# Optimization experiments

Measured on AMD Instinct MI355X. Metric: run time of the kernel, lower is better.

The kernel has to match this reference:

```python
import jax, jax.numpy as jnp
import numpy as np

B, S, D, H = 2, 2048, 1024, 16
DH = D // H          # 64, even -> RoPE valid
ROPE_BASE = 10000.0
LN_EPS = 1e-5


def _rope_cache(seq_len, head_dim, dtype):
    half = head_dim // 2
    inv_freq = 1.0 / (ROPE_BASE ** (jnp.arange(half, dtype=jnp.float32) / half))
    t = jnp.arange(seq_len, dtype=jnp.float32)
    freqs = t[:, None] * inv_freq[None, :]            # [S, half]
    emb = jnp.concatenate([freqs, freqs], axis=-1)    # [S, DH]
    return jnp.cos(emb).astype(dtype)[None, None], jnp.sin(emb).astype(dtype)[None, None]


def _rotate_every_two(x):
    x_even = x[..., ::2]
    x_odd = x[..., 1::2]
    return jnp.stack([-x_odd, x_even], axis=-1).reshape(x.shape)


def setup_inputs() -> dict:
    key = jax.random.key(0)
    ks = jax.random.split(key, 4)
    w = lambda k, shape: (jax.random.normal(k, shape, jnp.float32) * 0.02)
    return {
        "x_qk": jax.random.normal(ks[0], (B, S, D), jnp.float32),
        "x_v": jax.random.normal(ks[1], (B, S, D), jnp.float32),
        "W_qk": w(ks[2], (D, 2 * D)),
        "b_qk": jnp.zeros((2 * D,), jnp.float32),
        "W_v": w(ks[3], (D, D)),
        "b_v": jnp.zeros((D,), jnp.float32),
        "ln_gamma": jnp.ones((D,), jnp.float32),
        "ln_beta": jnp.zeros((D,), jnp.float32),
    }


def reference(x_qk, x_v, W_qk, b_qk, W_v, b_v, ln_gamma, ln_beta):
    b, s, d = x_qk.shape
    # fused QK projection -> [B,S,2,H,DH]
    qk = (x_qk @ W_qk + b_qk).reshape(b, s, 2, H, DH)
    q = jnp.transpose(qk[:, :, 0], (0, 2, 1, 3))  # [B,H,S,DH]
    k = jnp.transpose(qk[:, :, 1], (0, 2, 1, 3))
    v = jnp.transpose((x_v @ W_v + b_v).reshape(b, s, H, DH), (0, 2, 1, 3))

    cos, sin = _rope_cache(s, DH, q.dtype)
    q = q * cos + _rotate_every_two(q) * sin
    k = k * cos + _rotate_every_two(k) * sin

    scale = 1.0 / jnp.sqrt(jnp.asarray(DH, q.dtype))
    scores = jnp.einsum("bhqd,bhkd->bhqk", q, k) * scale
    probs = jax.nn.softmax(scores, axis=-1)
    attn = jnp.einsum("bhqk,bhkd->bhqd", probs, v)      # [B,H,S,DH]
    attn = jnp.transpose(attn, (0, 2, 1, 3)).reshape(b, s, d)

    mu = jnp.mean(attn, axis=-1, keepdims=True)
    var = jnp.var(attn, axis=-1, keepdims=True)
    out = (attn - mu) * jax.lax.rsqrt(var + LN_EPS) * ln_gamma + ln_beta
    return out
```

## Files before the change

kernel.cpp:

```cpp
#include <hip/hip_runtime.h>
#include <hip/hip_bf16.h>

#define Bn 2
#define Sn 2048
#define Dn 1024
#define Hn 16
#define DHn 64
#define Kd 1024
#define Mn (Bn * Sn)
#define LN10K 9.210340371976184f

typedef __attribute__((ext_vector_type(8))) short bf16x8;
typedef __attribute__((ext_vector_type(4))) float f32x4;
typedef __attribute__((ext_vector_type(16))) float f32x16;

static __device__ __forceinline__ ushort f2bf(float f) {
    uint u = __float_as_uint(f);
    u += 0x7fff + ((u >> 16) & 1);
    return (ushort)(u >> 16);
}
static __device__ __forceinline__ uint cvtpk(float a, float b) {
    uint r;
    asm("v_cvt_pk_bf16_f32 %0, %1, %2" : "=v"(r) : "v"(a), "v"(b));
    return r;
}
static __device__ __forceinline__ void plswap(uint& a, uint& b) {
    asm volatile("v_permlane32_swap_b32 %0, %1" : "+v"(a), "+v"(b));
}

#define MFMA16(a, b, c) __builtin_amdgcn_mfma_f32_16x16x32_bf16((a), (b), (c), 0, 0, 0)
#define MFMA32(a, b, c) __builtin_amdgcn_mfma_f32_32x32x16_bf16((a), (b), (c), 0, 0, 0)

static __device__ __forceinline__ void gload16(const ushort* g, ushort* l) {
    __builtin_amdgcn_global_load_lds(
        (const __attribute__((address_space(1))) void*)g,
        (__attribute__((address_space(3))) void*)l, 16, 0, 0);
}

static __device__ __forceinline__ int swz(int row, int col16) {
    return row * 128 + (((col16) * 16) ^ ((row & 7) << 4));
}

__global__ __launch_bounds__(256) void prep(
    const float* __restrict__ x_qk, const float* __restrict__ x_v,
    const float* __restrict__ W_qk, const float* __restrict__ W_v,
    ushort* __restrict__ xqkB, ushort* __restrict__ xvB,
    ushort* __restrict__ WqkT, ushort* __restrict__ WvT,
    float* __restrict__ ct, float* __restrict__ st)
{
    __shared__ ushort tle[32][33];
    const int blk = blockIdx.x;
    const int tid = threadIdx.x;

    if (blk < 4096) {
        const float* in = (blk < 2048) ? x_qk : x_v;
        ushort* out = (blk < 2048) ? xqkB : xvB;
        const int lb = (blk < 2048) ? blk : blk - 2048;
        const size_t i = ((size_t)lb * 256 + tid) * 8;
        const float4 a = *(const float4*)(in + i);
        const float4 b = *(const float4*)(in + i + 4);
        *(ushort4*)(out + i) =
            make_ushort4(f2bf(a.x), f2bf(a.y), f2bf(a.z), f2bf(a.w));
        *(ushort4*)(out + i + 4) =
            make_ushort4(f2bf(b.x), f2bf(b.y), f2bf(b.z), f2bf(b.w));
    } else if (blk < 7168) {
        const bool isQK = blk < 6144;
        const int t = isQK ? blk - 4096 : blk - 6144;
        const int C = isQK ? 2048 : 1024;
        const float* in = isQK ? W_qk : W_v;
        ushort* out = isQK ? WqkT : WvT;
        const int n0 = (isQK ? (t & 63) : (t & 31)) * 32;
        const int k0 = (isQK ? (t >> 6) : (t >> 5)) * 32;
        const int x = tid & 31, y = tid >> 5;
#pragma unroll
        for (int i = 0; i < 4; ++i)
            tle[y + 8 * i][x] = f2bf(in[(size_t)(k0 + y + 8 * i) * C + n0 + x]);
        __syncthreads();
#pragma unroll
        for (int i = 0; i < 4; ++i)
            out[(size_t)(n0 + y + 8 * i) * Kd + k0 + x] = tle[x][y + 8 * i];
    } else {
        const int idx = (blk - 7168) * 256 + tid;
        const int s = idx >> 5, fe = idx & 31;
        const float f = expf(-LN10K * (float)fe / 32.0f);
        const float a = (float)s * f;
        ct[idx] = cosf(a);
        st[idx] = sinf(a);
    }
}

__global__ __launch_bounds__(256) void gemm_fused_all(
    const ushort* __restrict__ xqkB, const ushort* __restrict__ xvB,
    const ushort* __restrict__ WqkT, const ushort* __restrict__ WvT,
    const float* __restrict__ b_qk, const float* __restrict__ b_v,
    const float* __restrict__ ctab, const float* __restrict__ stab,
    ushort* __restrict__ Qw, ushort* __restrict__ Kw, ushort* __restrict__ Vtw)
{
    __shared__ ushort Asm[128 * 64];
    __shared__ ushort Bsm[128 * 64];

    const bool isQK = blockIdx.x < 16;
    const ushort* A  = isQK ? xqkB : xvB;
    const ushort* Bt = isQK ? WqkT : WvT;
    const float* bias = isQK ? b_qk : b_v;
    const int nbase = (isQK ? blockIdx.x : blockIdx.x - 16) * 128;
    const int mbase = blockIdx.y * 128;

    const int tid = threadIdx.x;
    const int lane = tid & 63, w = tid >> 6;
    const int g = lane >> 4, c = lane & 15;
    const int wm = (w >> 1) * 64, wn = (w & 1) * 64;

    f32x4 acc[4][4];
#pragma unroll
    for (int mf = 0; mf < 4; ++mf)
#pragma unroll
        for (int nf = 0; nf < 4; ++nf)
            acc[mf][nf] = (f32x4){0.f, 0.f, 0.f, 0.f};

    const int sbase = w * 64 + lane;

    for (int k0 = 0; k0 < Kd; k0 += 64) {
#pragma unroll
        for (int j = 0; j < 4; ++j) {
            const int i = j * 256 + sbase;
            const int row = i >> 3, c16 = i & 7;
            const int kc = (c16 ^ (row & 7)) * 8;
            gload16(A + (size_t)(mbase + row) * Kd + k0 + kc,
                    &Asm[(size_t)(j * 256 + w * 64) * 8]);
            gload16(Bt + (size_t)(nbase + row) * Kd + k0 + kc,
                    &Bsm[(size_t)(j * 256 + w * 64) * 8]);
        }
        __syncthreads();

#pragma unroll
        for (int ks = 0; ks < 2; ++ks) {
            bf16x8 af[4], bfr[4];
#pragma unroll
            for (int mf = 0; mf < 4; ++mf) {
                const int row = wm + mf * 16 + c;
                af[mf] = *(const bf16x8*)((const char*)Asm + swz(row, ks * 4 + g));
            }
#pragma unroll
            for (int nf = 0; nf < 4; ++nf) {
                const int row = wn + nf * 16 + c;
                bfr[nf] = *(const bf16x8*)((const char*)Bsm + swz(row, ks * 4 + g));
            }
#pragma unroll
            for (int mf = 0; mf < 4; ++mf)
#pragma unroll
                for (int nf = 0; nf < 4; ++nf)
                    acc[mf][nf] = MFMA16(af[mf], bfr[nf], acc[mf][nf]);
        }
        __syncthreads();
    }

#pragma unroll
    for (int nf = 0; nf < 4; ++nf) {
        const int col = nbase + wn + nf * 16 + c;
        const float bs = bias[col];
        if (isQK) {
            const int dh = col & 63, h = (col >> 6) & 15, isK = col >> 10;
            ushort* dst = isK ? Kw : Qw;
            const float sc = isK ? 1.0f : 0.18033688011112042f;
            const float* cr = ctab + (dh & 31);
            const float* sr = stab + (dh & 31);
#pragma unroll
            for (int mf = 0; mf < 4; ++mf) {
#pragma unroll
                for (int r = 0; r < 4; ++r) {
                    const int row = mbase + wm + mf * 16 + g * 4 + r;
                    const int s = row & 2047, b = row >> 11;
                    const float v = acc[mf][nf][r] + bs;
                    const float p = __shfl_xor(v, 1);
                    const float cs = cr[s * 32], sn = sr[s * 32];
                    const float ov = (c & 1) ? v * cs + p * sn
                                             : v * cs - p * sn;
                    dst[(((size_t)(b * Hn + h)) * Sn + s) * DHn + dh] =
                        f2bf(ov * sc);
                }
            }
        } else {
            const int h = col >> 6, dh = col & 63;
#pragma unroll
            for (int mf = 0; mf < 4; ++mf) {
#pragma unroll
                for (int r = 0; r < 4; ++r) {
                    const int row = mbase + wm + mf * 16 + g * 4 + r;
                    const int s = row & 2047, b = row >> 11;
                    const float v = acc[mf][nf][r] + bs;
                    Vtw[(((size_t)(b * Hn + h)) * DHn + dh) * Sn + s] = f2bf(v);
                }
            }
        }
    }
}

__global__ __launch_bounds__(256) void attn_mfma(
    const ushort* __restrict__ Qg, const ushort* __restrict__ Kg,
    const ushort* __restrict__ Vtg, float* __restrict__ Aw)
{
    __shared__ char Kt[3][8192];
    __shared__ char Vt[3][8192];

    const int tid = threadIdx.x;
    const int lane = tid & 63, w = tid >> 6;
    const int r31 = lane & 31, hi = lane >> 5;
    const int bh = blockIdx.y;
    const int b = bh >> 4, h = bh & 15;
    const int q0 = blockIdx.x * 128 + w * 32;

    const ushort* qp = Qg + ((size_t)bh * Sn + q0 + r31) * DHn + hi * 8;
    bf16x8 qf[4];
#pragma unroll
    for (int kt = 0; kt < 4; ++kt)
        qf[kt] = *(const bf16x8*)(qp + kt * 16);

    const ushort* Kb = Kg + (size_t)bh * Sn * DHn;
    const ushort* Vb = Vtg + (size_t)bh * DHn * Sn;

    auto stage = [&](int buf, int kb) {
#pragma unroll
        for (int j = 0; j < 2; ++j) {
            const int i = j * 256 + w * 64 + lane;
            const int row = i >> 3, c16 = i & 7;
            const int kc = (c16 ^ (row & 7)) * 8;
            gload16(Kb + (size_t)(kb + row) * DHn + kc,
                    (ushort*)&Kt[buf][(j * 256 + w * 64) * 16]);
            gload16(Vb + (size_t)row * Sn + kb + kc,
                    (ushort*)&Vt[buf][(j * 256 + w * 64) * 16]);
        }
    };

    stage(0, 0);
    stage(1, 64);

    f32x16 acc0, acc1;
#pragma unroll
    for (int i = 0; i < 16; ++i) { acc0[i] = 0.f; acc1[i] = 0.f; }
    float m = -1e30f, lp = 0.f;

    const int NT = Sn / 64;
    for (int t = 0; t < NT; ++t) {
        const int cur = t % 3;

        if (t < NT - 1) {
            asm volatile("s_waitcnt vmcnt(4)" ::: "memory");
        } else {
            asm volatile("s_waitcnt vmcnt(0)" ::: "memory");
        }
        __builtin_amdgcn_sched_barrier(0);
        __builtin_amdgcn_s_barrier();
        __builtin_amdgcn_sched_barrier(0);

        f32x16 C0, C1;
#pragma unroll
        for (int i = 0; i < 16; ++i) { C0[i] = 0.f; C1[i] = 0.f; }
        __builtin_amdgcn_s_setprio(1);
#pragma unroll
        for (int kt = 0; kt < 4; ++kt) {
            const bf16x8 ka = *(const bf16x8*)&Kt[cur][swz(r31, kt * 2 + hi)];
            C0 = MFMA32(ka, qf[kt], C0);
        }
#pragma unroll
        for (int kt = 0; kt < 4; ++kt) {
            const bf16x8 ka = *(const bf16x8*)&Kt[cur][swz(32 + r31, kt * 2 + hi)];
            C1 = MFMA32(ka, qf[kt], C1);
        }
        __builtin_amdgcn_s_setprio(0);

        float mx[8];
#pragma unroll
        for (int i = 0; i < 8; ++i)
            mx[i] = fmaxf(fmaxf(C0[i], C0[i + 8]), fmaxf(C1[i], C1[i + 8]));
        mx[0] = fmaxf(mx[0], mx[4]); mx[1] = fmaxf(mx[1], mx[5]);
        mx[2] = fmaxf(mx[2], mx[6]); mx[3] = fmaxf(mx[3], mx[7]);
        float pmax = fmaxf(fmaxf(mx[0], mx[1]), fmaxf(mx[2], mx[3]));
        pmax = fmaxf(pmax, __shfl_xor(pmax, 32));

        if (__any(pmax > m + 11.5f)) {
            const float mn = fmaxf(m, pmax);
            const float a = exp2f(m - mn);
            m = mn;
            lp *= a;
#pragma unroll
            for (int reg = 0; reg < 16; ++reg) {
                const int qr = (reg & 3) + 8 * (reg >> 2) + 4 * hi;
                const float ar = __shfl(a, qr);
                acc0[reg] *= ar;
                acc1[reg] *= ar;
            }
        }

        bf16x8 paf[4];
#pragma unroll
        for (int tile = 0; tile < 2; ++tile) {
            const f32x16& C = tile ? C1 : C0;
            float e[16];
#pragma unroll
            for (int i = 0; i < 16; ++i) e[i] = exp2f(C[i] - m);
            float s = 0.f;
#pragma unroll
            for (int i = 0; i < 16; ++i) s += e[i];
            lp += s;
            uint p01 = cvtpk(e[0], e[1]),  p23 = cvtpk(e[2], e[3]);
            uint p45 = cvtpk(e[4], e[5]),  p67 = cvtpk(e[6], e[7]);
            uint p89 = cvtpk(e[8], e[9]),  pab = cvtpk(e[10], e[11]);
            uint pcd = cvtpk(e[12], e[13]), pef = cvtpk(e[14], e[15]);
            plswap(p01, p45); plswap(p23, p67);
            plswap(p89, pcd); plswap(pab, pef);
            uint4 f0 = {p01, p23, p45, p67};
            uint4 f1 = {p89, pab, pcd, pef};
            paf[tile * 2 + 0] = *(const bf16x8*)&f0;
            paf[tile * 2 + 1] = *(const bf16x8*)&f1;
        }

        __builtin_amdgcn_s_setprio(1);
#pragma unroll
        for (int kf = 0; kf < 4; ++kf) {
            const bf16x8 v0 = *(const bf16x8*)&Vt[cur][swz(r31, kf * 2 + hi)];
            acc0 = MFMA32(paf[kf], v0, acc0);
        }
#pragma unroll
        for (int kf = 0; kf < 4; ++kf) {
            const bf16x8 v1 = *(const bf16x8*)&Vt[cur][swz(32 + r31, kf * 2 + hi)];
            acc1 = MFMA32(paf[kf], v1, acc1);
        }
        __builtin_amdgcn_s_setprio(0);

        __builtin_amdgcn_sched_barrier(0);
        if (t + 2 < NT) stage((t + 2) % 3, (t + 2) * 64);
    }

    const float lv = lp + __shfl_xor(lp, 32);
    const float inv = 1.0f / lv;
#pragma unroll
    for (int reg = 0; reg < 16; ++reg) {
        const int qr = (reg & 3) + 8 * (reg >> 2) + 4 * hi;
        const float ir = __shfl(inv, qr);
        const int qs = q0 + qr;
        float* dst = &Aw[((size_t)b * Sn + qs) * Dn + h * DHn + r31];
        dst[0]  = acc0[reg] * ir;
        dst[32] = acc1[reg] * ir;
    }
}

__global__ __launch_bounds__(256) void ln_kernel(
    const float* __restrict__ Aw, const float* __restrict__ gamma,
    const float* __restrict__ beta, float* __restrict__ out)
{
    const int row = blockIdx.x;
    const int tid = threadIdx.x;
    const int d0 = tid * 4;
    const float4 x = *(const float4*)&Aw[(size_t)row * Dn + d0];
    float sum = x.x + x.y + x.z + x.w;
    float sq = x.x * x.x + x.y * x.y + x.z * x.z + x.w * x.w;
    for (int off = 32; off; off >>= 1) {
        sum += __shfl_xor(sum, off);
        sq += __shfl_xor(sq, off);
    }
    __shared__ float red[8];
    const int lane = tid & 63, wave = tid >> 6;
    if (lane == 0) { red[wave] = sum; red[wave + 4] = sq; }
    __syncthreads();
    if (tid == 0) {
        red[0] = red[0] + red[1] + red[2] + red[3];
        red[4] = red[4] + red[5] + red[6] + red[7];
    }
    __syncthreads();
    sum = red[0]; sq = red[4];
    const float mu = sum * (1.0f / Dn);
    const float var = sq * (1.0f / Dn) - mu * mu;
    const float rs = rsqrtf(var + 1e-5f);

    const float4 gv = *(const float4*)&gamma[d0];
    const float4 bv = *(const float4*)&beta[d0];
    float4 ov;
    ov.x = (x.x - mu) * rs * gv.x + bv.x;
    ov.y = (x.y - mu) * rs * gv.y + bv.y;
    ov.z = (x.z - mu) * rs * gv.z + bv.z;
    ov.w = (x.w - mu) * rs * gv.w + bv.w;
    *(float4*)&out[(size_t)row * Dn + d0] = ov;
}

extern "C" void kernel_launch(void* const* d_in, const int* in_sizes, int n_in,
                              void* d_out, int out_size, void* d_ws, size_t ws_size,
                              hipStream_t stream)
{
    const float* x_qk = (const float*)d_in[0];
    const float* x_v  = (const float*)d_in[1];
    const float* W_qk = (const float*)d_in[2];
    const float* b_qk = (const float*)d_in[3];
    const float* W_v  = (const float*)d_in[4];
    const float* b_v  = (const float*)d_in[5];
    const float* g    = (const float*)d_in[6];
    const float* be   = (const float*)d_in[7];

    char* ws = (char*)d_ws;
    ushort* Qw    = (ushort*)(ws);
    ushort* Kw    = (ushort*)(ws + (8u  << 20));
    ushort* Vtw   = (ushort*)(ws + (16u << 20));
    float*  Aw    = (float*) (ws + (24u << 20));
    ushort* xqkB  = (ushort*)(ws + (40u << 20));
    ushort* xvB   = (ushort*)(ws + (48u << 20));
    ushort* WqkT  = (ushort*)(ws + (56u << 20));
    ushort* WvT   = (ushort*)(ws + (60u << 20));
    float*  ctab  = (float*) (ws + (62u << 20));
    float*  stab  = (float*) (ws + (62u << 20) + (256u << 10));

    prep<<<7424, 256, 0, stream>>>(x_qk, x_v, W_qk, W_v,
                                   xqkB, xvB, WqkT, WvT, ctab, stab);
    gemm_fused_all<<<dim3(24, 32), 256, 0, stream>>>(
        xqkB, xvB, WqkT, WvT, b_qk, b_v, ctab, stab, Qw, Kw, Vtw);
    attn_mfma<<<dim3(16, 32), 256, 0, stream>>>(Qw, Kw, Vtw, Aw);
    ln_kernel<<<Bn * Sn, 256, 0, stream>>>(Aw, g, be, (float*)d_out);
}
```

Baseline: 137.6 us.

## Split attention KV range across two blocks and merge partials in LayerNorm

The attention grid gains a z dimension that splits the key/value sequence in half, doubling the block count so the GPU has more parallel work. Each half writes unnormalized bf16 partial outputs plus per-row max and sum, and the LayerNorm kernel merges them with log-sum-exp weights before normalizing. Other changes ride along: the row sum is now computed by an MFMA against a vector of ones, the pipeline drops from triple to double buffering with a plain __syncthreads, and the setprio hints are removed. The costs are extra partial-result traffic, bf16 rounding of the partials, and a shorter pipeline that may expose more load latency.

```diff
diff --git a/kernel.cpp b/kernel.cpp
--- a/kernel.cpp
+++ b/kernel.cpp
@@ -18,6 +18,9 @@
     uint u = __float_as_uint(f);
     u += 0x7fff + ((u >> 16) & 1);
     return (ushort)(u >> 16);
+}
+static __device__ __forceinline__ float bf2f(ushort u) {
+    return __uint_as_float(((uint)u) << 16);
 }
 static __device__ __forceinline__ uint cvtpk(float a, float b) {
     uint r;
@@ -196,12 +199,14 @@
     }
 }
 
-__global__ __launch_bounds__(256) void attn_mfma(
+__global__ __launch_bounds__(256, 4) void attn_mfma(
     const ushort* __restrict__ Qg, const ushort* __restrict__ Kg,
-    const ushort* __restrict__ Vtg, float* __restrict__ Aw)
+    const ushort* __restrict__ Vtg, ushort* __restrict__ OP0,
+    ushort* __restrict__ OP1, float* __restrict__ L0, float* __restrict__ M0,
+    float* __restrict__ L1, float* __restrict__ M1)
 {
-    __shared__ char Kt[3][8192];
-    __shared__ char Vt[3][8192];
+    __shared__ char Kt[2][8192];
+    __shared__ char Vt[2][8192];
 
     const int tid = threadIdx.x;
     const int lane = tid & 63, w = tid >> 6;
@@ -209,12 +214,22 @@
     const int bh = blockIdx.y;
     const int b = bh >> 4, h = bh & 15;
     const int q0 = blockIdx.x * 128 + w * 32;
+    const int half = blockIdx.z;
+    const int kvb = half * (Sn / 2);
+
+    ushort* __restrict__ OP = half ? OP1 : OP0;
+    float* __restrict__ Lh = half ? L1 : L0;
+    float* __restrict__ Mh = half ? M1 : M0;
 
     const ushort* qp = Qg + ((size_t)bh * Sn + q0 + r31) * DHn + hi * 8;
     bf16x8 qf[4];
 #pragma unroll
     for (int kt = 0; kt < 4; ++kt)
         qf[kt] = *(const bf16x8*)(qp + kt * 16);
+
+    const short one_bf = (short)0x3F80;
+    const bf16x8 ones = {one_bf, one_bf, one_bf, one_bf,
+                         one_bf, one_bf, one_bf, one_bf};
 
     const ushort* Kb = Kg + (size_t)bh * Sn * DHn;
     const ushort* Vb = Vtg + (size_t)bh * DHn * Sn;
@@ -232,42 +247,43 @@
         }
     };
 
-    stage(0, 0);
-    stage(1, 64);
-
-    f32x16 acc0, acc1;
-#pragma unroll
-    for (int i = 0; i < 16; ++i) { acc0[i] = 0.f; acc1[i] = 0.f; }
-    float m = -1e30f, lp = 0.f;
-
-    const int NT = Sn / 64;
+    stage(0, kvb);
+
+    f32x16 acc0, acc1, lacc;
+#pragma unroll
+    for (int i = 0; i < 16; ++i) { acc0[i] = 0.f; acc1[i] = 0.f; lacc[i] = 0.f; }
+    float m = -1e30f;
+    f32x16 zzv;
+#pragma unroll
+    for (int i = 0; i < 16; ++i) zzv[i] = 0.f;
+
+    const int NT = (Sn / 2) / 64;
     for (int t = 0; t < NT; ++t) {
-        const int cur = t % 3;
-
-        if (t < NT - 1) {
-            asm volatile("s_waitcnt vmcnt(4)" ::: "memory");
-        } else {
-            asm volatile("s_waitcnt vmcnt(0)" ::: "memory");
-        }
+        const int cur = t & 1;
+
+        __syncthreads();
+        if (t + 1 < NT) stage(cur ^ 1, kvb + (t + 1) * 64);
         __builtin_amdgcn_sched_barrier(0);
-        __builtin_amdgcn_s_barrier();
-        __builtin_amdgcn_sched_barrier(0);
 
         f32x16 C0, C1;
-#pragma unroll
-        for (int i = 0; i < 16; ++i) { C0[i] = 0.f; C1[i] = 0.f; }
-        __builtin_amdgcn_s_setprio(1);
-#pragma unroll
-        for (int kt = 0; kt < 4; ++kt) {
+        {
+            const bf16x8 ka0 = *(const bf16x8*)&Kt[cur][swz(r31, hi)];
+            C0 = MFMA32(ka0, qf[0], zzv);
+        }
+#pragma unroll
+        for (int kt = 1; kt < 4; ++kt) {
             const bf16x8 ka = *(const bf16x8*)&Kt[cur][swz(r31, kt * 2 + hi)];
             C0 = MFMA32(ka, qf[kt], C0);
         }
-#pragma unroll
-        for (int kt = 0; kt < 4; ++kt) {
+        {
+            const bf16x8 ka0 = *(const bf16x8*)&Kt[cur][swz(32 + r31, hi)];
+            C1 = MFMA32(ka0, qf[0], zzv);
+        }
+#pragma unroll
+        for (int kt = 1; kt < 4; ++kt) {
             const bf16x8 ka = *(const bf16x8*)&Kt[cur][swz(32 + r31, kt * 2 + hi)];
             C1 = MFMA32(ka, qf[kt], C1);
         }
-        __builtin_amdgcn_s_setprio(0);
 
         float mx[8];
 #pragma unroll
@@ -282,13 +298,13 @@
             const float mn = fmaxf(m, pmax);
             const float a = exp2f(m - mn);
             m = mn;
-            lp *= a;
 #pragma unroll
             for (int reg = 0; reg < 16; ++reg) {
                 const int qr = (reg & 3) + 8 * (reg >> 2) + 4 * hi;
                 const float ar = __shfl(a, qr);
                 acc0[reg] *= ar;
                 acc1[reg] *= ar;
+                lacc[reg] *= ar;
             }
         }
 
@@ -299,10 +315,6 @@
             float e[16];
 #pragma unroll
             for (int i = 0; i < 16; ++i) e[i] = exp2f(C[i] - m);
-            float s = 0.f;
-#pragma unroll
-            for (int i = 0; i < 16; ++i) s += e[i];
-            lp += s;
             uint p01 = cvtpk(e[0], e[1]),  p23 = cvtpk(e[2], e[3]);
             uint p45 = cvtpk(e[4], e[5]),  p67 = cvtpk(e[6], e[7]);
             uint p89 = cvtpk(e[8], e[9]),  pab = cvtpk(e[10], e[11]);
@@ -315,7 +327,6 @@
             paf[tile * 2 + 1] = *(const bf16x8*)&f1;
         }
 
-        __builtin_amdgcn_s_setprio(1);
 #pragma unroll
         for (int kf = 0; kf < 4; ++kf) {
             const bf16x8 v0 = *(const bf16x8*)&Vt[cur][swz(r31, kf * 2 + hi)];
@@ -326,33 +337,58 @@
             const bf16x8 v1 = *(const bf16x8*)&Vt[cur][swz(32 + r31, kf * 2 + hi)];
             acc1 = MFMA32(paf[kf], v1, acc1);
         }
-        __builtin_amdgcn_s_setprio(0);
-
-        __builtin_amdgcn_sched_barrier(0);
-        if (t + 2 < NT) stage((t + 2) % 3, (t + 2) * 64);
-    }
-
-    const float lv = lp + __shfl_xor(lp, 32);
-    const float inv = 1.0f / lv;
+#pragma unroll
+        for (int kf = 0; kf < 4; ++kf)
+            lacc = MFMA32(paf[kf], ones, lacc);
+    }
+
 #pragma unroll
     for (int reg = 0; reg < 16; ++reg) {
         const int qr = (reg & 3) + 8 * (reg >> 2) + 4 * hi;
-        const float ir = __shfl(inv, qr);
         const int qs = q0 + qr;
-        float* dst = &Aw[((size_t)b * Sn + qs) * Dn + h * DHn + r31];
-        dst[0]  = acc0[reg] * ir;
-        dst[32] = acc1[reg] * ir;
-    }
-}
-
-__global__ __launch_bounds__(256) void ln_kernel(
-    const float* __restrict__ Aw, const float* __restrict__ gamma,
-    const float* __restrict__ beta, float* __restrict__ out)
+        ushort* dst = &OP[((size_t)b * Sn + qs) * Dn + h * DHn + r31];
+        dst[0]  = f2bf(acc0[reg]);
+        dst[32] = f2bf(acc1[reg]);
+    }
+    if (r31 == 0) {
+#pragma unroll
+        for (int reg = 0; reg < 16; ++reg) {
+            const int qr = (reg & 3) + 8 * (reg >> 2) + 4 * hi;
+            Lh[(size_t)bh * Sn + q0 + qr] = lacc[reg];
+        }
+    }
+    if (hi == 0)
+        Mh[(size_t)bh * Sn + q0 + r31] = m;
+}
+
+__global__ __launch_bounds__(256) void ln_combine(
+    const ushort* __restrict__ OP0, const ushort* __restrict__ OP1,
+    const float* __restrict__ L0, const float* __restrict__ M0,
+    const float* __restrict__ L1, const float* __restrict__ M1,
+    const float* __restrict__ gamma, const float* __restrict__ beta,
+    float* __restrict__ out)
 {
     const int row = blockIdx.x;
+    const int b = row >> 11, s = row & 2047;
     const int tid = threadIdx.x;
     const int d0 = tid * 4;
-    const float4 x = *(const float4*)&Aw[(size_t)row * Dn + d0];
+    const int h = d0 >> 6;
+    const size_t idx = (size_t)(b * Hn + h) * Sn + s;
+
+    const float l0 = L0[idx], m0 = M0[idx];
+    const float l1 = L1[idx], m1 = M1[idx];
+    const float mm = fmaxf(m0, m1);
+    const float w0 = exp2f(m0 - mm), w1 = exp2f(m1 - mm);
+    const float inv = 1.0f / (l0 * w0 + l1 * w1);
+
+    const ushort4 u0 = *(const ushort4*)&OP0[(size_t)row * Dn + d0];
+    const ushort4 u1 = *(const ushort4*)&OP1[(size_t)row * Dn + d0];
+    float4 x;
+    x.x = (bf2f(u0.x) * w0 + bf2f(u1.x) * w1) * inv;
+    x.y = (bf2f(u0.y) * w0 + bf2f(u1.y) * w1) * inv;
+    x.z = (bf2f(u0.z) * w0 + bf2f(u1.z) * w1) * inv;
+    x.w = (bf2f(u0.w) * w0 + bf2f(u1.w) * w1) * inv;
+
     float sum = x.x + x.y + x.z + x.w;
     float sq = x.x * x.x + x.y * x.y + x.z * x.z + x.w * x.w;
     for (int off = 32; off; off >>= 1) {
@@ -400,11 +436,16 @@
     ushort* Qw    = (ushort*)(ws);
     ushort* Kw    = (ushort*)(ws + (8u  << 20));
     ushort* Vtw   = (ushort*)(ws + (16u << 20));
-    float*  Aw    = (float*) (ws + (24u << 20));
+    ushort* OP0   = (ushort*)(ws + (24u << 20));
+    ushort* OP1   = (ushort*)(ws + (32u << 20));
     ushort* xqkB  = (ushort*)(ws + (40u << 20));
     ushort* xvB   = (ushort*)(ws + (48u << 20));
     ushort* WqkT  = (ushort*)(ws + (56u << 20));
     ushort* WvT   = (ushort*)(ws + (60u << 20));
+    float*  L0    = (float*) (ws + (56u << 20));
+    float*  M0    = L0 + 65536;
+    float*  L1    = M0 + 65536;
+    float*  M1    = L1 + 65536;
     float*  ctab  = (float*) (ws + (62u << 20));
     float*  stab  = (float*) (ws + (62u << 20) + (256u << 10));
 
@@ -412,6 +453,8 @@
                                    xqkB, xvB, WqkT, WvT, ctab, stab);
     gemm_fused_all<<<dim3(24, 32), 256, 0, stream>>>(
         xqkB, xvB, WqkT, WvT, b_qk, b_v, ctab, stab, Qw, Kw, Vtw);
-    attn_mfma<<<dim3(16, 32), 256, 0, stream>>>(Qw, Kw, Vtw, Aw);
-    ln_kernel<<<Bn * Sn, 256, 0, stream>>>(Aw, g, be, (float*)d_out);
-}
+    attn_mfma<<<dim3(16, 32, 2), 256, 0, stream>>>(
+        Qw, Kw, Vtw, OP0, OP1, L0, M0, L1, M1);
+    ln_combine<<<Bn * Sn, 256, 0, stream>>>(OP0, OP1, L0, M0, L1, M1,
+                                            g, be, (float*)d_out);
+}
```

After: 149.5 us. +8.7%, slower.

## Use 128-key attention tiles with double buffering instead of 64-key triple buffering

Applied to the files above, without the earlier changes.

The attention kernel now processes 128 keys per iteration, with four score MFMA tiles and eight PV k-steps. It uses two 16KB LDS buffers per K/V and issues the prefetch for the next tile right after the barrier, replacing the 3-stage pipeline. This halves the number of barriers and softmax max/rescale rounds per query block. In exchange it raises register pressure (four score accumulators, eight P fragments) and waits on all outstanding loads every iteration. The s_setprio hints are also removed.

```diff
diff --git a/kernel.cpp b/kernel.cpp
--- a/kernel.cpp
+++ b/kernel.cpp
@@ -39,6 +39,9 @@
 
 static __device__ __forceinline__ int swz(int row, int col16) {
     return row * 128 + (((col16) * 16) ^ ((row & 7) << 4));
+}
+static __device__ __forceinline__ int swzV(int row, int col16) {
+    return row * 256 + (((col16) * 16) ^ ((row & 7) << 4));
 }
 
 __global__ __launch_bounds__(256) void prep(
@@ -200,8 +203,8 @@
     const ushort* __restrict__ Qg, const ushort* __restrict__ Kg,
     const ushort* __restrict__ Vtg, float* __restrict__ Aw)
 {
-    __shared__ char Kt[3][8192];
-    __shared__ char Vt[3][8192];
+    __shared__ char Kt[2][16384];
+    __shared__ char Vt[2][16384];
 
     const int tid = threadIdx.x;
     const int lane = tid & 63, w = tid >> 6;
@@ -221,42 +224,38 @@
 
     auto stage = [&](int buf, int kb) {
 #pragma unroll
-        for (int j = 0; j < 2; ++j) {
+        for (int j = 0; j < 4; ++j) {
             const int i = j * 256 + w * 64 + lane;
-            const int row = i >> 3, c16 = i & 7;
-            const int kc = (c16 ^ (row & 7)) * 8;
-            gload16(Kb + (size_t)(kb + row) * DHn + kc,
+            const int krow = i >> 3, kc16 = i & 7;
+            gload16(Kb + (size_t)(kb + krow) * DHn + ((kc16 ^ (krow & 7)) * 8),
                     (ushort*)&Kt[buf][(j * 256 + w * 64) * 16]);
-            gload16(Vb + (size_t)row * Sn + kb + kc,
+            const int vrow = i >> 4, vc16 = i & 15;
+            gload16(Vb + (size_t)vrow * Sn + kb + ((vc16 ^ (vrow & 7)) * 8),
                     (ushort*)&Vt[buf][(j * 256 + w * 64) * 16]);
         }
     };
 
     stage(0, 0);
-    stage(1, 64);
 
     f32x16 acc0, acc1;
 #pragma unroll
     for (int i = 0; i < 16; ++i) { acc0[i] = 0.f; acc1[i] = 0.f; }
     float m = -1e30f, lp = 0.f;
 
-    const int NT = Sn / 64;
+    const int NT = Sn / 128;
     for (int t = 0; t < NT; ++t) {
-        const int cur = t % 3;
-
-        if (t < NT - 1) {
-            asm volatile("s_waitcnt vmcnt(4)" ::: "memory");
-        } else {
-            asm volatile("s_waitcnt vmcnt(0)" ::: "memory");
-        }
+        const int cur = t & 1;
+
+        asm volatile("s_waitcnt vmcnt(0)" ::: "memory");
         __builtin_amdgcn_sched_barrier(0);
         __builtin_amdgcn_s_barrier();
         __builtin_amdgcn_sched_barrier(0);
-
-        f32x16 C0, C1;
-#pragma unroll
-        for (int i = 0; i < 16; ++i) { C0[i] = 0.f; C1[i] = 0.f; }
-        __builtin_amdgcn_s_setprio(1);
+        if (t + 1 < NT) stage(cur ^ 1, (t + 1) * 128);
+        __builtin_amdgcn_sched_barrier(0);
+
+        f32x16 C0, C1, C2, C3;
+#pragma unroll
+        for (int i = 0; i < 16; ++i) { C0[i] = 0.f; C1[i] = 0.f; C2[i] = 0.f; C3[i] = 0.f; }
 #pragma unroll
         for (int kt = 0; kt < 4; ++kt) {
             const bf16x8 ka = *(const bf16x8*)&Kt[cur][swz(r31, kt * 2 + hi)];
@@ -267,12 +266,24 @@
             const bf16x8 ka = *(const bf16x8*)&Kt[cur][swz(32 + r31, kt * 2 + hi)];
             C1 = MFMA32(ka, qf[kt], C1);
         }
-        __builtin_amdgcn_s_setprio(0);
+#pragma unroll
+        for (int kt = 0; kt < 4; ++kt) {
+            const bf16x8 ka = *(const bf16x8*)&Kt[cur][swz(64 + r31, kt * 2 + hi)];
+            C2 = MFMA32(ka, qf[kt], C2);
+        }
+#pragma unroll
+        for (int kt = 0; kt < 4; ++kt) {
+            const bf16x8 ka = *(const bf16x8*)&Kt[cur][swz(96 + r31, kt * 2 + hi)];
+            C3 = MFMA32(ka, qf[kt], C3);
+        }
 
         float mx[8];
 #pragma unroll
-        for (int i = 0; i < 8; ++i)
-            mx[i] = fmaxf(fmaxf(C0[i], C0[i + 8]), fmaxf(C1[i], C1[i + 8]));
+        for (int i = 0; i < 8; ++i) {
+            float a01 = fmaxf(fmaxf(C0[i], C0[i + 8]), fmaxf(C1[i], C1[i + 8]));
+            float a23 = fmaxf(fmaxf(C2[i], C2[i + 8]), fmaxf(C3[i], C3[i + 8]));
+            mx[i] = fmaxf(a01, a23);
+        }
         mx[0] = fmaxf(mx[0], mx[4]); mx[1] = fmaxf(mx[1], mx[5]);
         mx[2] = fmaxf(mx[2], mx[6]); mx[3] = fmaxf(mx[3], mx[7]);
         float pmax = fmaxf(fmaxf(mx[0], mx[1]), fmaxf(mx[2], mx[3]));
@@ -292,44 +303,42 @@
             }
         }
 
-        bf16x8 paf[4];
-#pragma unroll
-        for (int tile = 0; tile < 2; ++tile) {
-            const f32x16& C = tile ? C1 : C0;
-            float e[16];
-#pragma unroll
-            for (int i = 0; i < 16; ++i) e[i] = exp2f(C[i] - m);
-            float s = 0.f;
-#pragma unroll
-            for (int i = 0; i < 16; ++i) s += e[i];
-            lp += s;
-            uint p01 = cvtpk(e[0], e[1]),  p23 = cvtpk(e[2], e[3]);
-            uint p45 = cvtpk(e[4], e[5]),  p67 = cvtpk(e[6], e[7]);
-            uint p89 = cvtpk(e[8], e[9]),  pab = cvtpk(e[10], e[11]);
-            uint pcd = cvtpk(e[12], e[13]), pef = cvtpk(e[14], e[15]);
-            plswap(p01, p45); plswap(p23, p67);
-            plswap(p89, pcd); plswap(pab, pef);
-            uint4 f0 = {p01, p23, p45, p67};
-            uint4 f1 = {p89, pab, pcd, pef};
-            paf[tile * 2 + 0] = *(const bf16x8*)&f0;
-            paf[tile * 2 + 1] = *(const bf16x8*)&f1;
-        }
-
-        __builtin_amdgcn_s_setprio(1);
-#pragma unroll
-        for (int kf = 0; kf < 4; ++kf) {
-            const bf16x8 v0 = *(const bf16x8*)&Vt[cur][swz(r31, kf * 2 + hi)];
+        bf16x8 paf[8];
+        {
+            const f32x16* Cs[4] = {&C0, &C1, &C2, &C3};
+#pragma unroll
+            for (int tile = 0; tile < 4; ++tile) {
+                const f32x16& C = *Cs[tile];
+                float e[16];
+#pragma unroll
+                for (int i = 0; i < 16; ++i) e[i] = exp2f(C[i] - m);
+                float s = 0.f;
+#pragma unroll
+                for (int i = 0; i < 16; ++i) s += e[i];
+                lp += s;
+                uint p01 = cvtpk(e[0], e[1]),  p23 = cvtpk(e[2], e[3]);
+                uint p45 = cvtpk(e[4], e[5]),  p67 = cvtpk(e[6], e[7]);
+                uint p89 = cvtpk(e[8], e[9]),  pab = cvtpk(e[10], e[11]);
+                uint pcd = cvtpk(e[12], e[13]), pef = cvtpk(e[14], e[15]);
+                plswap(p01, p45); plswap(p23, p67);
+                plswap(p89, pcd); plswap(pab, pef);
+                uint4 f0 = {p01, p23, p45, p67};
+                uint4 f1 = {p89, pab, pcd, pef};
+                paf[tile * 2 + 0] = *(const bf16x8*)&f0;
+                paf[tile * 2 + 1] = *(const bf16x8*)&f1;
+            }
+        }
+
+#pragma unroll
+        for (int kf = 0; kf < 8; ++kf) {
+            const bf16x8 v0 = *(const bf16x8*)&Vt[cur][swzV(r31, kf * 2 + hi)];
             acc0 = MFMA32(paf[kf], v0, acc0);
         }
 #pragma unroll
-        for (int kf = 0; kf < 4; ++kf) {
-            const bf16x8 v1 = *(const bf16x8*)&Vt[cur][swz(32 + r31, kf * 2 + hi)];
+        for (int kf = 0; kf < 8; ++kf) {
+            const bf16x8 v1 = *(const bf16x8*)&Vt[cur][swzV(32 + r31, kf * 2 + hi)];
             acc1 = MFMA32(paf[kf], v1, acc1);
         }
-        __builtin_amdgcn_s_setprio(0);
-
-        __builtin_amdgcn_sched_barrier(0);
-        if (t + 2 < NT) stage((t + 2) % 3, (t + 2) * 64);
     }
 
     const float lv = lp + __shfl_xor(lp, 32);
```

Result: slower. 163.9 us (+19.1%).
